# Performance work log

Hardware: AMD Instinct MI355X
Metric: run time of the kernel (lower is better)

## Reference

```python
import jax, jax.numpy as jnp
import numpy as np

LN_EPS = 1e-5
NORM_EPS = 1e-12
SLOPE = 0.1

def _layernorm(x, g, b):
    m = jnp.mean(x, axis=-1, keepdims=True)
    v = jnp.mean(jnp.square(x - m), axis=-1, keepdims=True)
    return (x - m) * jax.lax.rsqrt(v + LN_EPS) * g + b

def _leaky(x):
    return jnp.where(x >= 0, x, SLOPE * x)

def setup_inputs() -> dict:
    key = jax.random.key(0)
    ks = jax.random.split(key, 8)
    N = 1048576
    features = jax.random.normal(ks[0], (N, 128), dtype=jnp.float32)
    # PyTorch Linear default init: U(-1/sqrt(fan_in), 1/sqrt(fan_in))
    W1 = jax.random.uniform(ks[1], (32, 128), jnp.float32, -1/np.sqrt(128), 1/np.sqrt(128))
    g1 = jnp.ones((32,), jnp.float32); b1 = jnp.zeros((32,), jnp.float32)
    W2 = jax.random.uniform(ks[2], (16, 32), jnp.float32, -1/np.sqrt(32), 1/np.sqrt(32))
    g2 = jnp.ones((16,), jnp.float32); b2 = jnp.zeros((16,), jnp.float32)
    W3 = jax.random.uniform(ks[3], (3, 16), jnp.float32, -1/np.sqrt(16), 1/np.sqrt(16))
    b3 = jax.random.uniform(ks[4], (3,), jnp.float32, -1/np.sqrt(16), 1/np.sqrt(16))
    return {"features": features, "W1": W1, "g1": g1, "b1": b1,
            "W2": W2, "g2": g2, "b2": b2, "W3": W3, "b3": b3}

def reference(features, W1, g1, b1, W2, g2, b2, W3, b3):
    x = features @ W1.T                       # [N,32]
    x = _leaky(_layernorm(x, g1, b1))
    x = x @ W2.T                               # [N,16]
    x = _leaky(_layernorm(x, g2, b2))
    x = x @ W3.T + b3                          # [N,3]
    # F.normalize(dim=-1): x / max(||x||_2, eps)
    n = jnp.linalg.norm(x, axis=-1, keepdims=True)
    return x / jnp.maximum(n, NORM_EPS)
```

## Files before the change

kernel.cpp:

```cpp
#include <hip/hip_runtime.h>
#include <math.h>

typedef short bf16x8 __attribute__((ext_vector_type(8)));
typedef float f32x4  __attribute__((ext_vector_type(4)));
typedef float f32x2  __attribute__((ext_vector_type(2)));

#define TPB 256
#define CSTRIDE 36
#define BFR_BYTES 16384
#define CT_BYTES (256 * CSTRIDE * 4)
#define BOFF(nt, ks, p) ((((nt)*4 + (ks))*2 + (p))*256)

#define PKFMA(a, b, c) __builtin_elementwise_fma((a), (b), (c))

__device__ __forceinline__ unsigned cvt_pk_bf16(float lo, float hi) {
    unsigned r;
    asm("v_cvt_pk_bf16_f32 %0, %1, %2" : "=v"(r) : "v"(lo), "v"(hi));
    return r;
}
__device__ __forceinline__ void split2pk(float x0, float x1, unsigned &p, unsigned &q) {
    p = cvt_pk_bf16(x0, x1);
    f32x2 xv = {x0, x1};
    f32x2 fv = {__uint_as_float(p << 16), __uint_as_float(p & 0xffff0000u)};
    f32x2 r = xv - fv;
    q = cvt_pk_bf16(r.x, r.y);
}
__device__ __forceinline__ f32x2 leaky2(f32x2 y) {
    const f32x2 zero = {0.f, 0.f};
    const f32x2 slope = {0.1f, 0.1f};
    return PKFMA(__builtin_elementwise_min(y, zero), slope,
                 __builtin_elementwise_max(y, zero));
}

__global__ __launch_bounds__(TPB, 3) void decoder_kernel(
    const float* __restrict__ feat,
    const float* __restrict__ W1, const float* __restrict__ g1, const float* __restrict__ b1,
    const float* __restrict__ W2, const float* __restrict__ g2, const float* __restrict__ b2,
    const float* __restrict__ W3, const float* __restrict__ b3,
    float* __restrict__ out, int N)
{
    __shared__ __align__(16) unsigned char lds[BFR_BYTES + CT_BYTES];
    unsigned* bfr = (unsigned*)lds;

    const int t = threadIdx.x;
    const int l = t & 63;
    const int w = t >> 6;
    const int arow = l & 15;
    const int acol = (l >> 4) * 8;
    float* myCt = (float*)(lds + BFR_BYTES) + w * 64 * CSTRIDE;

    const size_t rows0 = (size_t)blockIdx.x * 256 + (size_t)w * 64;

    float4 buf[2][8];
    {
        size_t rr = rows0 + arow;
        if (rr >= (size_t)N) rr = N - 1;
        const float* ap = feat + rr * 128 + acol;
#pragma unroll
        for (int ks = 0; ks < 4; ++ks) {
            buf[0][2 * ks]     = *(const float4*)(ap + ks * 32);
            buf[0][2 * ks + 1] = *(const float4*)(ap + ks * 32 + 4);
        }
    }

    for (int c = t; c < 512; c += 256) {
        const int lc = c & 63, ks = (c >> 6) & 3, nt = (c >> 8) & 1;
        const float* wp = W1 + (nt * 16 + (lc & 15)) * 128 + ks * 32 + (lc >> 4) * 8;
        float v[8];
        *(float4*)(v)     = *(const float4*)(wp);
        *(float4*)(v + 4) = *(const float4*)(wp + 4);
        unsigned p[4], q[4];
#pragma unroll
        for (int i = 0; i < 4; ++i) split2pk(v[2*i], v[2*i+1], p[i], q[i]);
        uint4 q1 = {p[0], p[1], p[2], p[3]};
        uint4 q2 = {q[0], q[1], q[2], q[3]};
        *(uint4*)(bfr + BOFF(nt, ks, 0) + lc * 4) = q1;
        *(uint4*)(bfr + BOFF(nt, ks, 1) + lc * 4) = q2;
    }
    __syncthreads();

#pragma unroll
    for (int j = 0; j < 4; ++j) {
        if (j < 3) {
            size_t rr = rows0 + (j + 1) * 16 + arow;
            if (rr >= (size_t)N) rr = N - 1;
            const float* ap = feat + rr * 128 + acol;
#pragma unroll
            for (int ks = 0; ks < 4; ++ks) {
                buf[(j + 1) & 1][2 * ks]     = *(const float4*)(ap + ks * 32);
                buf[(j + 1) & 1][2 * ks + 1] = *(const float4*)(ap + ks * 32 + 4);
            }
        }
        f32x4 acc0 = {0.f, 0.f, 0.f, 0.f};
        f32x4 acc1 = {0.f, 0.f, 0.f, 0.f};
#pragma unroll
        for (int ks = 0; ks < 4; ++ks) {
            float v[8];
            *(float4*)(v)     = buf[j & 1][2 * ks];
            *(float4*)(v + 4) = buf[j & 1][2 * ks + 1];
            unsigned p[4], q[4];
#pragma unroll
            for (int i = 0; i < 4; ++i) split2pk(v[2*i], v[2*i+1], p[i], q[i]);
            uint4 q1 = {p[0], p[1], p[2], p[3]};
            uint4 q2 = {q[0], q[1], q[2], q[3]};
            bf16x8 a1 = __builtin_bit_cast(bf16x8, q1);
            bf16x8 a2 = __builtin_bit_cast(bf16x8, q2);
            bf16x8 B10 = __builtin_bit_cast(bf16x8, *(const uint4*)(bfr + BOFF(0, ks, 0) + l * 4));
            bf16x8 B20 = __builtin_bit_cast(bf16x8, *(const uint4*)(bfr + BOFF(0, ks, 1) + l * 4));
            bf16x8 B11 = __builtin_bit_cast(bf16x8, *(const uint4*)(bfr + BOFF(1, ks, 0) + l * 4));
            bf16x8 B21 = __builtin_bit_cast(bf16x8, *(const uint4*)(bfr + BOFF(1, ks, 1) + l * 4));
            acc0 = __builtin_amdgcn_mfma_f32_16x16x32_bf16(a1, B10, acc0, 0, 0, 0);
            acc1 = __builtin_amdgcn_mfma_f32_16x16x32_bf16(a1, B11, acc1, 0, 0, 0);
            acc0 = __builtin_amdgcn_mfma_f32_16x16x32_bf16(a2, B10, acc0, 0, 0, 0);
            acc1 = __builtin_amdgcn_mfma_f32_16x16x32_bf16(a2, B11, acc1, 0, 0, 0);
            acc0 = __builtin_amdgcn_mfma_f32_16x16x32_bf16(a1, B20, acc0, 0, 0, 0);
            acc1 = __builtin_amdgcn_mfma_f32_16x16x32_bf16(a1, B21, acc1, 0, 0, 0);
        }
        const int crow = j * 16 + (l >> 4) * 4;
        const int ccol = l & 15;
#pragma unroll
        for (int r = 0; r < 4; ++r) {
            myCt[(crow + r) * CSTRIDE + ccol]      = acc0[r];
            myCt[(crow + r) * CSTRIDE + 16 + ccol] = acc1[r];
        }
    }

    f32x2 xp[16];
#pragma unroll
    for (int c = 0; c < 8; ++c) {
        const float4 v = *(const float4*)(myCt + l * CSTRIDE + c * 4);
        xp[2 * c]     = f32x2{v.x, v.y};
        xp[2 * c + 1] = f32x2{v.z, v.w};
    }

    f32x2 sv = xp[0];
#pragma unroll
    for (int i = 1; i < 16; ++i) sv += xp[i];
    const float m = (sv.x + sv.y) * (1.f / 32.f);
    const f32x2 mv = {m, m};
    f32x2 vv = {0.f, 0.f};
#pragma unroll
    for (int i = 0; i < 16; ++i) { const f32x2 d = xp[i] - mv; vv = PKFMA(d, d, vv); }
    const float rs1 = rsqrtf((vv.x + vv.y) * (1.f / 32.f) + 1e-5f);
    const f32x2 rs1v = {rs1, rs1};

    f32x2 zp[16];
#pragma unroll
    for (int i = 0; i < 16; ++i) {
        const f32x2 gb = *(const f32x2*)(g1 + 2 * i);
        const f32x2 bb = *(const f32x2*)(b1 + 2 * i);
        zp[i] = leaky2(PKFMA((xp[i] - mv) * rs1v, gb, bb));
    }

    float a2v[16];
#pragma unroll
    for (int k = 0; k < 16; ++k) {
        const float* __restrict__ wrow = W2 + k * 32;
        f32x2 acc = {0.f, 0.f};
#pragma unroll
        for (int jj = 0; jj < 16; ++jj)
            acc = PKFMA(zp[jj], *(const f32x2*)(wrow + 2 * jj), acc);
        a2v[k] = acc.x + acc.y;
    }

    f32x2 a2p[8];
#pragma unroll
    for (int i = 0; i < 8; ++i) a2p[i] = f32x2{a2v[2 * i], a2v[2 * i + 1]};

    f32x2 s2 = a2p[0];
#pragma unroll
    for (int i = 1; i < 8; ++i) s2 += a2p[i];
    const float m2 = (s2.x + s2.y) * (1.f / 16.f);
    const f32x2 m2v = {m2, m2};
    f32x2 v2v = {0.f, 0.f};
#pragma unroll
    for (int i = 0; i < 8; ++i) { const f32x2 d = a2p[i] - m2v; v2v = PKFMA(d, d, v2v); }
    const float rs2 = rsqrtf((v2v.x + v2v.y) * (1.f / 16.f) + 1e-5f);
    const f32x2 rs2v = {rs2, rs2};

    f32x2 z2p[8];
#pragma unroll
    for (int i = 0; i < 8; ++i) {
        const f32x2 gb = *(const f32x2*)(g2 + 2 * i);
        const f32x2 bb = *(const f32x2*)(b2 + 2 * i);
        z2p[i] = leaky2(PKFMA((a2p[i] - m2v) * rs2v, gb, bb));
    }

    float o[3];
#pragma unroll
    for (int q = 0; q < 3; ++q) {
        const float* __restrict__ wrow = W3 + q * 16;
        f32x2 acc = {0.f, 0.f};
#pragma unroll
        for (int jj = 0; jj < 8; ++jj)
            acc = PKFMA(z2p[jj], *(const f32x2*)(wrow + 2 * jj), acc);
        o[q] = b3[q] + acc.x + acc.y;
    }
    const float nrm = sqrtf(o[0]*o[0] + o[1]*o[1] + o[2]*o[2]);
    const float inv = 1.f / fmaxf(nrm, 1e-12f);

    const size_t myrow = rows0 + l;
    if (myrow < (size_t)N) {
        out[myrow * 3 + 0] = o[0] * inv;
        out[myrow * 3 + 1] = o[1] * inv;
        out[myrow * 3 + 2] = o[2] * inv;
    }
}

extern "C" void kernel_launch(void* const* d_in, const int* in_sizes, int n_in,
                              void* d_out, int out_size, void* d_ws, size_t ws_size,
                              hipStream_t stream) {
    const float* feat = (const float*)d_in[0];
    const float* W1   = (const float*)d_in[1];
    const float* g1   = (const float*)d_in[2];
    const float* b1   = (const float*)d_in[3];
    const float* W2   = (const float*)d_in[4];
    const float* g2   = (const float*)d_in[5];
    const float* b2   = (const float*)d_in[6];
    const float* W3   = (const float*)d_in[7];
    const float* b3   = (const float*)d_in[8];
    float* out = (float*)d_out;

    const int N = in_sizes[0] / 128;
    const int grid = (N + 255) / 256;

    decoder_kernel<<<grid, TPB, 0, stream>>>(feat, W1, g1, b1, W2, g2, b2, W3, b3, out, N);
}
```

Measured before the change: 118.8 us.

## Convert decoder kernel to persistent grid-stride loop with cross-chunk prefetch

```diff
diff --git a/kernel.cpp b/kernel.cpp
--- a/kernel.cpp
+++ b/kernel.cpp
@@ -6,6 +6,7 @@
 typedef float f32x2  __attribute__((ext_vector_type(2)));
 
 #define TPB 256
+#define GRID 768
 #define CSTRIDE 36
 #define BFR_BYTES 16384
 #define CT_BYTES (256 * CSTRIDE * 4)
@@ -32,12 +33,24 @@
                  __builtin_elementwise_max(y, zero));
 }
 
+__device__ __forceinline__ void load_tile(float4* dst, const float* __restrict__ feat,
+                                          unsigned rbase, int arow, int acol, unsigned nm1) {
+    unsigned rr = rbase + arow;
+    rr = rr < nm1 ? rr : nm1;
+    const float* ap = feat + (size_t)rr * 128 + acol;
+#pragma unroll
+    for (int ks = 0; ks < 4; ++ks) {
+        dst[2 * ks]     = *(const float4*)(ap + ks * 32);
+        dst[2 * ks + 1] = *(const float4*)(ap + ks * 32 + 4);
+    }
+}
+
 __global__ __launch_bounds__(TPB, 3) void decoder_kernel(
     const float* __restrict__ feat,
     const float* __restrict__ W1, const float* __restrict__ g1, const float* __restrict__ b1,
     const float* __restrict__ W2, const float* __restrict__ g2, const float* __restrict__ b2,
     const float* __restrict__ W3, const float* __restrict__ b3,
-    float* __restrict__ out, int N)
+    float* __restrict__ out, int N, unsigned nchunks)
 {
     __shared__ __align__(16) unsigned char lds[BFR_BYTES + CT_BYTES];
     unsigned* bfr = (unsigned*)lds;
@@ -47,24 +60,18 @@
     const int w = t >> 6;
     const int arow = l & 15;
     const int acol = (l >> 4) * 8;
+    const unsigned nm1 = (unsigned)(N - 1);
     float* myCt = (float*)(lds + BFR_BYTES) + w * 64 * CSTRIDE;
 
-    const size_t rows0 = (size_t)blockIdx.x * 256 + (size_t)w * 64;
+    const unsigned wid = blockIdx.x * 4 + w;
+    const unsigned NW  = GRID * 4;
 
     float4 buf[2][8];
-    {
-        size_t rr = rows0 + arow;
-        if (rr >= (size_t)N) rr = N - 1;
-        const float* ap = feat + rr * 128 + acol;
-#pragma unroll
-        for (int ks = 0; ks < 4; ++ks) {
-            buf[0][2 * ks]     = *(const float4*)(ap + ks * 32);
-            buf[0][2 * ks + 1] = *(const float4*)(ap + ks * 32 + 4);
-        }
-    }
-
-    for (int c = t; c < 512; c += 256) {
-        const int lc = c & 63, ks = (c >> 6) & 3, nt = (c >> 8) & 1;
+    unsigned c = wid;
+    if (c < nchunks) load_tile(buf[0], feat, c * 64, arow, acol, nm1);
+
+    for (int cc = t; cc < 512; cc += 256) {
+        const int lc = cc & 63, ks = (cc >> 6) & 3, nt = (cc >> 8) & 1;
         const float* wp = W1 + (nt * 16 + (lc & 15)) * 128 + ks * 32 + (lc >> 4) * 8;
         float v[8];
         *(float4*)(v)     = *(const float4*)(wp);
@@ -79,131 +86,132 @@
     }
     __syncthreads();
 
-#pragma unroll
-    for (int j = 0; j < 4; ++j) {
-        if (j < 3) {
-            size_t rr = rows0 + (j + 1) * 16 + arow;
-            if (rr >= (size_t)N) rr = N - 1;
-            const float* ap = feat + rr * 128 + acol;
+    for (; c < nchunks; c += NW) {
+        const unsigned base = c * 64;
+
+#pragma unroll
+        for (int j = 0; j < 4; ++j) {
+            if (j < 3) {
+                load_tile(buf[(j + 1) & 1], feat, base + (j + 1) * 16, arow, acol, nm1);
+            } else {
+                const unsigned cn = c + NW;
+                if (cn < nchunks)
+                    load_tile(buf[0], feat, cn * 64, arow, acol, nm1);
+            }
+            f32x4 acc0 = {0.f, 0.f, 0.f, 0.f};
+            f32x4 acc1 = {0.f, 0.f, 0.f, 0.f};
 #pragma unroll
             for (int ks = 0; ks < 4; ++ks) {
-                buf[(j + 1) & 1][2 * ks]     = *(const float4*)(ap + ks * 32);
-                buf[(j + 1) & 1][2 * ks + 1] = *(const float4*)(ap + ks * 32 + 4);
+                float v[8];
+                *(float4*)(v)     = buf[j & 1][2 * ks];
+                *(float4*)(v + 4) = buf[j & 1][2 * ks + 1];
+                unsigned p[4], q[4];
+#pragma unroll
+                for (int i = 0; i < 4; ++i) split2pk(v[2*i], v[2*i+1], p[i], q[i]);
+                uint4 q1 = {p[0], p[1], p[2], p[3]};
+                uint4 q2 = {q[0], q[1], q[2], q[3]};
+                bf16x8 a1 = __builtin_bit_cast(bf16x8, q1);
+                bf16x8 a2 = __builtin_bit_cast(bf16x8, q2);
+                bf16x8 B10 = __builtin_bit_cast(bf16x8, *(const uint4*)(bfr + BOFF(0, ks, 0) + l * 4));
+                bf16x8 B20 = __builtin_bit_cast(bf16x8, *(const uint4*)(bfr + BOFF(0, ks, 1) + l * 4));
+                bf16x8 B11 = __builtin_bit_cast(bf16x8, *(const uint4*)(bfr + BOFF(1, ks, 0) + l * 4));
+                bf16x8 B21 = __builtin_bit_cast(bf16x8, *(const uint4*)(bfr + BOFF(1, ks, 1) + l * 4));
+                acc0 = __builtin_amdgcn_mfma_f32_16x16x32_bf16(a1, B10, acc0, 0, 0, 0);
+                acc1 = __builtin_amdgcn_mfma_f32_16x16x32_bf16(a1, B11, acc1, 0, 0, 0);
+                acc0 = __builtin_amdgcn_mfma_f32_16x16x32_bf16(a2, B10, acc0, 0, 0, 0);
+                acc1 = __builtin_amdgcn_mfma_f32_16x16x32_bf16(a2, B11, acc1, 0, 0, 0);
+                acc0 = __builtin_amdgcn_mfma_f32_16x16x32_bf16(a1, B20, acc0, 0, 0, 0);
+                acc1 = __builtin_amdgcn_mfma_f32_16x16x32_bf16(a1, B21, acc1, 0, 0, 0);
             }
-        }
-        f32x4 acc0 = {0.f, 0.f, 0.f, 0.f};
-        f32x4 acc1 = {0.f, 0.f, 0.f, 0.f};
-#pragma unroll
-        for (int ks = 0; ks < 4; ++ks) {
-            float v[8];
-            *(float4*)(v)     = buf[j & 1][2 * ks];
-            *(float4*)(v + 4) = buf[j & 1][2 * ks + 1];
-            unsigned p[4], q[4];
-#pragma unroll
-            for (int i = 0; i < 4; ++i) split2pk(v[2*i], v[2*i+1], p[i], q[i]);
-            uint4 q1 = {p[0], p[1], p[2], p[3]};
-            uint4 q2 = {q[0], q[1], q[2], q[3]};
-            bf16x8 a1 = __builtin_bit_cast(bf16x8, q1);
-            bf16x8 a2 = __builtin_bit_cast(bf16x8, q2);
-            bf16x8 B10 = __builtin_bit_cast(bf16x8, *(const uint4*)(bfr + BOFF(0, ks, 0) + l * 4));
-            bf16x8 B20 = __builtin_bit_cast(bf16x8, *(const uint4*)(bfr + BOFF(0, ks, 1) + l * 4));
-            bf16x8 B11 = __builtin_bit_cast(bf16x8, *(const uint4*)(bfr + BOFF(1, ks, 0) + l * 4));
-            bf16x8 B21 = __builtin_bit_cast(bf16x8, *(const uint4*)(bfr + BOFF(1, ks, 1) + l * 4));
-            acc0 = __builtin_amdgcn_mfma_f32_16x16x32_bf16(a1, B10, acc0, 0, 0, 0);
-            acc1 = __builtin_amdgcn_mfma_f32_16x16x32_bf16(a1, B11, acc1, 0, 0, 0);
-            acc0 = __builtin_amdgcn_mfma_f32_16x16x32_bf16(a2, B10, acc0, 0, 0, 0);
-            acc1 = __builtin_amdgcn_mfma_f32_16x16x32_bf16(a2, B11, acc1, 0, 0, 0);
-            acc0 = __builtin_amdgcn_mfma_f32_16x16x32_bf16(a1, B20, acc0, 0, 0, 0);
-            acc1 = __builtin_amdgcn_mfma_f32_16x16x32_bf16(a1, B21, acc1, 0, 0, 0);
-        }
-        const int crow = j * 16 + (l >> 4) * 4;
-        const int ccol = l & 15;
-#pragma unroll
-        for (int r = 0; r < 4; ++r) {
-            myCt[(crow + r) * CSTRIDE + ccol]      = acc0[r];
-            myCt[(crow + r) * CSTRIDE + 16 + ccol] = acc1[r];
-        }
-    }
-
-    f32x2 xp[16];
-#pragma unroll
-    for (int c = 0; c < 8; ++c) {
-        const float4 v = *(const float4*)(myCt + l * CSTRIDE + c * 4);
-        xp[2 * c]     = f32x2{v.x, v.y};
-        xp[2 * c + 1] = f32x2{v.z, v.w};
-    }
-
-    f32x2 sv = xp[0];
-#pragma unroll
-    for (int i = 1; i < 16; ++i) sv += xp[i];
-    const float m = (sv.x + sv.y) * (1.f / 32.f);
-    const f32x2 mv = {m, m};
-    f32x2 vv = {0.f, 0.f};
-#pragma unroll
-    for (int i = 0; i < 16; ++i) { const f32x2 d = xp[i] - mv; vv = PKFMA(d, d, vv); }
-    const float rs1 = rsqrtf((vv.x + vv.y) * (1.f / 32.f) + 1e-5f);
-    const f32x2 rs1v = {rs1, rs1};
-
-    f32x2 zp[16];
-#pragma unroll
-    for (int i = 0; i < 16; ++i) {
-        const f32x2 gb = *(const f32x2*)(g1 + 2 * i);
-        const f32x2 bb = *(const f32x2*)(b1 + 2 * i);
-        zp[i] = leaky2(PKFMA((xp[i] - mv) * rs1v, gb, bb));
-    }
-
-    float a2v[16];
-#pragma unroll
-    for (int k = 0; k < 16; ++k) {
-        const float* __restrict__ wrow = W2 + k * 32;
-        f32x2 acc = {0.f, 0.f};
-#pragma unroll
-        for (int jj = 0; jj < 16; ++jj)
-            acc = PKFMA(zp[jj], *(const f32x2*)(wrow + 2 * jj), acc);
-        a2v[k] = acc.x + acc.y;
-    }
-
-    f32x2 a2p[8];
-#pragma unroll
-    for (int i = 0; i < 8; ++i) a2p[i] = f32x2{a2v[2 * i], a2v[2 * i + 1]};
-
-    f32x2 s2 = a2p[0];
-#pragma unroll
-    for (int i = 1; i < 8; ++i) s2 += a2p[i];
-    const float m2 = (s2.x + s2.y) * (1.f / 16.f);
-    const f32x2 m2v = {m2, m2};
-    f32x2 v2v = {0.f, 0.f};
-#pragma unroll
-    for (int i = 0; i < 8; ++i) { const f32x2 d = a2p[i] - m2v; v2v = PKFMA(d, d, v2v); }
-    const float rs2 = rsqrtf((v2v.x + v2v.y) * (1.f / 16.f) + 1e-5f);
-    const f32x2 rs2v = {rs2, rs2};
-
-    f32x2 z2p[8];
-#pragma unroll
-    for (int i = 0; i < 8; ++i) {
-        const f32x2 gb = *(const f32x2*)(g2 + 2 * i);
-        const f32x2 bb = *(const f32x2*)(b2 + 2 * i);
-        z2p[i] = leaky2(PKFMA((a2p[i] - m2v) * rs2v, gb, bb));
-    }
-
-    float o[3];
-#pragma unroll
-    for (int q = 0; q < 3; ++q) {
-        const float* __restrict__ wrow = W3 + q * 16;
-        f32x2 acc = {0.f, 0.f};
-#pragma unroll
-        for (int jj = 0; jj < 8; ++jj)
-            acc = PKFMA(z2p[jj], *(const f32x2*)(wrow + 2 * jj), acc);
-        o[q] = b3[q] + acc.x + acc.y;
-    }
-    const float nrm = sqrtf(o[0]*o[0] + o[1]*o[1] + o[2]*o[2]);
-    const float inv = 1.f / fmaxf(nrm, 1e-12f);
-
-    const size_t myrow = rows0 + l;
-    if (myrow < (size_t)N) {
-        out[myrow * 3 + 0] = o[0] * inv;
-        out[myrow * 3 + 1] = o[1] * inv;
-        out[myrow * 3 + 2] = o[2] * inv;
+            const int crow = j * 16 + (l >> 4) * 4;
+            const int ccol = l & 15;
+#pragma unroll
+            for (int r = 0; r < 4; ++r) {
+                myCt[(crow + r) * CSTRIDE + ccol]      = acc0[r];
+                myCt[(crow + r) * CSTRIDE + 16 + ccol] = acc1[r];
+            }
+        }
+
+        f32x2 xp[16];
+#pragma unroll
+        for (int cc = 0; cc < 8; ++cc) {
+            const float4 v = *(const float4*)(myCt + l * CSTRIDE + cc * 4);
+            xp[2 * cc]     = f32x2{v.x, v.y};
+            xp[2 * cc + 1] = f32x2{v.z, v.w};
+        }
+
+        f32x2 sv = xp[0];
+#pragma unroll
+        for (int i = 1; i < 16; ++i) sv += xp[i];
+        const float m = (sv.x + sv.y) * (1.f / 32.f);
+        const f32x2 mv = {m, m};
+        f32x2 vv = {0.f, 0.f};
+#pragma unroll
+        for (int i = 0; i < 16; ++i) { const f32x2 d = xp[i] - mv; vv = PKFMA(d, d, vv); }
+        const float rs1 = rsqrtf((vv.x + vv.y) * (1.f / 32.f) + 1e-5f);
+        const f32x2 rs1v = {rs1, rs1};
+
+        f32x2 zp[16];
+#pragma unroll
+        for (int i = 0; i < 16; ++i) {
+            const f32x2 gb = *(const f32x2*)(g1 + 2 * i);
+            const f32x2 bb = *(const f32x2*)(b1 + 2 * i);
+            zp[i] = leaky2(PKFMA((xp[i] - mv) * rs1v, gb, bb));
+        }
+
+        float a2v[16];
+#pragma unroll
+        for (int k = 0; k < 16; ++k) {
+            const float* __restrict__ wrow = W2 + k * 32;
+            f32x2 acc = {0.f, 0.f};
+#pragma unroll
+            for (int jj = 0; jj < 16; ++jj)
+                acc = PKFMA(zp[jj], *(const f32x2*)(wrow + 2 * jj), acc);
+            a2v[k] = acc.x + acc.y;
+        }
+
+        f32x2 a2p[8];
+#pragma unroll
+        for (int i = 0; i < 8; ++i) a2p[i] = f32x2{a2v[2 * i], a2v[2 * i + 1]};
+
+        f32x2 s2 = a2p[0];
+#pragma unroll
+        for (int i = 1; i < 8; ++i) s2 += a2p[i];
+        const float m2 = (s2.x + s2.y) * (1.f / 16.f);
+        const f32x2 m2v = {m2, m2};
+        f32x2 v2v = {0.f, 0.f};
+#pragma unroll
+        for (int i = 0; i < 8; ++i) { const f32x2 d = a2p[i] - m2v; v2v = PKFMA(d, d, v2v); }
+        const float rs2 = rsqrtf((v2v.x + v2v.y) * (1.f / 16.f) + 1e-5f);
+        const f32x2 rs2v = {rs2, rs2};
+
+        f32x2 z2p[8];
+#pragma unroll
+        for (int i = 0; i < 8; ++i) {
+            const f32x2 gb = *(const f32x2*)(g2 + 2 * i);
+            const f32x2 bb = *(const f32x2*)(b2 + 2 * i);
+            z2p[i] = leaky2(PKFMA((a2p[i] - m2v) * rs2v, gb, bb));
+        }
+
+        float o[3];
+#pragma unroll
+        for (int q = 0; q < 3; ++q) {
+            const float* __restrict__ wrow = W3 + q * 16;
+            f32x2 acc = {0.f, 0.f};
+#pragma unroll
+            for (int jj = 0; jj < 8; ++jj)
+                acc = PKFMA(z2p[jj], *(const f32x2*)(wrow + 2 * jj), acc);
+            o[q] = b3[q] + acc.x + acc.y;
+        }
+        const float nrm = sqrtf(o[0]*o[0] + o[1]*o[1] + o[2]*o[2]);
+        const float inv = 1.f / fmaxf(nrm, 1e-12f);
+
+        const size_t myrow = (size_t)base + l;
+        if (myrow < (size_t)N) {
+            out[myrow * 3 + 0] = o[0] * inv;
+            out[myrow * 3 + 1] = o[1] * inv;
+            out[myrow * 3 + 2] = o[2] * inv;
+        }
     }
 }
 
@@ -222,7 +230,8 @@
     float* out = (float*)d_out;
 
     const int N = in_sizes[0] / 128;
-    const int grid = (N + 255) / 256;
-
-    decoder_kernel<<<grid, TPB, 0, stream>>>(feat, W1, g1, b1, W2, g2, b2, W3, b3, out, N);
-}
+    const unsigned nchunks = (unsigned)((N + 63) / 64);
+
+    decoder_kernel<<<GRID, TPB, 0, stream>>>(feat, W1, g1, b1, W2, g2, b2, W3, b3,
+                                             out, N, nchunks);
+}
```

Result: faster. 112.7 us (-5.1%).
